# Kernel optimization log

Measured on AMD Instinct MI355X. Metric: run time of the kernel, lower is better.

The kernel has to match this reference:

```python
import jax, jax.numpy as jnp
import numpy as np

B, IN, COND, H, LAT, E, GH = 8192, 256, 1024, 1024, 128, 6, 64
INP = LAT + COND      # decoder layer0 input size = 1152
INTER = LAT + H       # decoder layer1/2 input size = 1152


def setup_inputs() -> dict:
    key = jax.random.key(0)
    ks = jax.random.split(key, 30)
    n = lambda k, shape, s=0.02: jax.random.normal(k, shape, dtype=jnp.float32) * s
    return {
        'x': jax.random.normal(ks[0], (B, IN), dtype=jnp.float32),
        'y': jax.random.normal(ks[1], (B, COND), dtype=jnp.float32),
        'eps': jax.random.normal(ks[2], (B, LAT), dtype=jnp.float32),
        # encoder: layer k input = prev_dim + IN (x is re-concatenated each layer)
        'enc_w0': n(ks[3], (IN + COND + IN, H)), 'enc_b0': jnp.zeros((H,), jnp.float32),
        'enc_w1': n(ks[4], (H + IN, H)),         'enc_b1': jnp.zeros((H,), jnp.float32),
        'mu_w': n(ks[5], (H, LAT)),  'mu_b': jnp.zeros((LAT,), jnp.float32),
        'lv_w': n(ks[6], (H, LAT)),  'lv_b': jnp.zeros((LAT,), jnp.float32),
        # gating network (input = latent + cond)
        'g_w0': n(ks[7], (INP, GH)), 'g_b0': jnp.zeros((GH,), jnp.float32),
        'g_w1': n(ks[8], (GH, GH)),  'g_b1': jnp.zeros((GH,), jnp.float32),
        'g_w2': n(ks[9], (GH, E)),   'g_b2': jnp.zeros((E,), jnp.float32),
        # expert weights [E, in, out] and biases [E, out] (bias init 0.01 as in source)
        'exp_w0': n(ks[10], (E, INP, H)),   'exp_b0': jnp.full((E, H), 0.01, jnp.float32),
        'exp_w1': n(ks[11], (E, INTER, H)), 'exp_b1': jnp.full((E, H), 0.01, jnp.float32),
        'exp_w2': n(ks[12], (E, INTER, IN)), 'exp_b2': jnp.full((E, IN), 0.01, jnp.float32),
    }


def _forward(x, y, eps, enc_w0, enc_b0, enc_w1, enc_b1, mu_w, mu_b, lv_w, lv_b,
             g_w0, g_b0, g_w1, g_b1, g_w2, g_b2,
             exp_w0, exp_b0, exp_w1, exp_b1, exp_w2, exp_b2):
    elu = jax.nn.elu
    # --- Encoder ---
    h = jnp.concatenate([x, y], axis=1)
    h = elu(jnp.concatenate([h, x], axis=1) @ enc_w0 + enc_b0)
    h = elu(jnp.concatenate([h, x], axis=1) @ enc_w1 + enc_b1)
    mu = h @ mu_w + mu_b
    logvar = h @ lv_w + lv_b
    # --- Reparameterize (eps passed explicitly for determinism) ---
    z = mu + eps * jnp.exp(0.5 * logvar)
    # --- MixedDecoder ---
    g = jnp.concatenate([z, y], axis=1)
    g = elu(g @ g_w0 + g_b0)
    g = elu(g @ g_w1 + g_b1)
    coeff = jax.nn.softmax(g @ g_w2 + g_b2, axis=1)  # [B, E]
    layer_out = y
    for W, bb, act in ((exp_w0, exp_b0, True), (exp_w1, exp_b1, True), (exp_w2, exp_b2, False)):
        inp = jnp.concatenate([z, layer_out], axis=1)  # [B, I]
        # fused mixture-of-experts projection: avoids materializing per-sample [B,I,O] weight
        out = coeff @ bb + jnp.einsum('be,bi,eio->bo', coeff, inp, W)
        layer_out = elu(out) if act else out
    return layer_out, mu, logvar


def reference(x, y, eps, enc_w0, enc_b0, enc_w1, enc_b1, mu_w, mu_b, lv_w, lv_b,
              g_w0, g_b0, g_w1, g_b1, g_w2, g_b2,
              exp_w0, exp_b0, exp_w1, exp_b1, exp_w2, exp_b2):
    return _forward(x, y, eps, enc_w0, enc_b0, enc_w1, enc_b1, mu_w, mu_b, lv_w, lv_b,
                    g_w0, g_b0, g_w1, g_b1, g_w2, g_b2,
                    exp_w0, exp_b0, exp_w1, exp_b1, exp_w2, exp_b2)
```

## Files before the change

### kernel.cpp

```cpp
#include <hip/hip_runtime.h>
#include <hip/hip_bf16.h>
#include <cstddef>

using u16 = unsigned short;
using short8 = __attribute__((ext_vector_type(8))) short;
using f32x4 = __attribute__((ext_vector_type(4))) float;

constexpr int B_   = 8192;
constexpr int IN_  = 256;
constexpr int COND_= 1024;
constexpr int H_   = 1024;
constexpr int LAT_ = 128;
constexpr int NE_  = 6;
constexpr int GH_  = 64;
constexpr int INP_ = 1152;
constexpr int K0_  = 1536;
constexpr int K1_  = 1280;

constexpr int BK = 64;

typedef const __attribute__((address_space(1))) void gv_t;
typedef __attribute__((address_space(3))) void lv_t;
#define GLDS(g, l) __builtin_amdgcn_global_load_lds((gv_t*)(g), (lv_t*)(l), 16, 0, 0)

__device__ __forceinline__ u16 f2b(float f) {
  __hip_bfloat16 h = __float2bfloat16(f);
  return *reinterpret_cast<u16*>(&h);
}
__device__ __forceinline__ float elu1(float x) { return x > 0.f ? x : (__expf(x) - 1.f); }

__global__ void k_transpose(const float* __restrict__ in, u16* __restrict__ out,
                            int R, int C, long inStride, long outStride) {
  __shared__ float t[32][33];
  const float* ip = in + (long)blockIdx.z * inStride;
  u16* op = out + (long)blockIdx.z * outStride;
  int c0 = blockIdx.x * 32, r0 = blockIdx.y * 32;
  int tx = threadIdx.x, ty = threadIdx.y;
#pragma unroll
  for (int i = 0; i < 4; i++) {
    int r = r0 + ty + i * 8, c = c0 + tx;
    if (r < R && c < C) t[ty + i * 8][tx] = ip[(long)r * C + c];
  }
  __syncthreads();
#pragma unroll
  for (int i = 0; i < 4; i++) {
    int c = c0 + ty + i * 8, r = r0 + tx;
    if (r < R && c < C) op[(long)c * R + r] = f2b(t[tx][ty + i * 8]);
  }
}

__global__ void k_prep(const float* __restrict__ x, const float* __restrict__ y,
                       u16* __restrict__ A0, u16* __restrict__ A1) {
  long idx = (long)blockIdx.x * blockDim.x + threadIdx.x;
  long n0 = (long)B_ * K0_;
  if (idx < n0) {
    int b = (int)(idx / K0_), c = (int)(idx % K0_);
    float v;
    if (c < IN_)            v = x[(long)b * IN_ + c];
    else if (c < IN_+COND_) v = y[(long)b * COND_ + (c - IN_)];
    else                    v = x[(long)b * IN_ + (c - IN_ - COND_)];
    A0[idx] = f2b(v);
  } else {
    long j = idx - n0;
    if (j < (long)B_ * IN_) {
      int b = (int)(j / IN_), c = (int)(j % IN_);
      A1[(long)b * K1_ + H_ + c] = f2b(x[(long)b * IN_ + c]);
    }
  }
}

__global__ void k_z(const float* __restrict__ mu, const float* __restrict__ lv,
                    const float* __restrict__ eps, const float* __restrict__ y,
                    u16* __restrict__ ZY, u16* __restrict__ D1, u16* __restrict__ D2) {
  long idx = (long)blockIdx.x * blockDim.x + threadIdx.x;
  if (idx >= (long)B_ * INP_) return;
  int b = (int)(idx / INP_), c = (int)(idx % INP_);
  if (c < LAT_) {
    long o = (long)b * LAT_ + c;
    float z = mu[o] + eps[o] * __expf(0.5f * lv[o]);
    u16 zb = f2b(z);
    ZY[idx] = zb; D1[idx] = zb; D2[idx] = zb;
  } else {
    ZY[idx] = f2b(y[(long)b * COND_ + (c - LAT_)]);
  }
}

__global__ __launch_bounds__(256) void k_gate(const float* __restrict__ G1,
    const float* __restrict__ w1, const float* __restrict__ b1,
    const float* __restrict__ w2, const float* __restrict__ b2,
    float* __restrict__ coeff) {
  __shared__ float W1[64][65];
  __shared__ float W2[64][8];
  __shared__ float B1[64], B2[8];
  int tid = threadIdx.x;
  for (int i = tid; i < 64 * 64; i += 256) W1[i >> 6][i & 63] = w1[i];
  for (int i = tid; i < 64 * 6; i += 256) W2[i / 6][i % 6] = w2[i];
  if (tid < 64) B1[tid] = b1[tid];
  if (tid < 8)  B2[tid] = (tid < 6) ? b2[tid] : 0.f;
  __syncthreads();
  int row = blockIdx.x * 256 + tid;
  const float* gr = G1 + (long)row * GH_;
  float g[64];
#pragma unroll
  for (int i = 0; i < 16; i++) {
    float4 v = *(const float4*)(gr + i * 4);
    g[i*4] = v.x; g[i*4+1] = v.y; g[i*4+2] = v.z; g[i*4+3] = v.w;
  }
  float lg[6];
#pragma unroll
  for (int e = 0; e < 6; e++) lg[e] = B2[e];
  for (int n = 0; n < 64; n++) {
    float s = B1[n];
#pragma unroll
    for (int k = 0; k < 64; k++) s += g[k] * W1[k][n];
    s = elu1(s);
#pragma unroll
    for (int e = 0; e < 6; e++) lg[e] += s * W2[n][e];
  }
  float m = lg[0];
#pragma unroll
  for (int e = 1; e < 6; e++) m = fmaxf(m, lg[e]);
  float p[6], sum = 0.f;
#pragma unroll
  for (int e = 0; e < 6; e++) { p[e] = __expf(lg[e] - m); sum += p[e]; }
  float inv = 1.f / sum;
#pragma unroll
  for (int e = 0; e < 6; e++) coeff[(long)row * 6 + e] = p[e] * inv;
}

template<int KSTEPS, int E, bool MOE>
__global__ __launch_bounds__(512, 2) void k_gemm8(
    const u16* __restrict__ A,
    const u16* __restrict__ WT,
    const float* __restrict__ bias,
    const float* __restrict__ coeff,
    int N,
    u16* __restrict__ outH, int ldo)
{
  constexpr int KK = KSTEPS * BK;
  constexpr int T = E * KSTEPS;
  __shared__ __align__(16) u16 As[3][256][BK];
  __shared__ __align__(16) u16 Bs[3][128][BK];
  __shared__ float Cf[MOE ? 256 : 1][8];

  const int tid = threadIdx.x;
  const int lane = tid & 63, w = tid >> 6;
  const int wr = w >> 1, wc = w & 1;
  const int lin = blockIdx.x + blockIdx.y * gridDim.x;
  const int rb  = (lin & 7) * 4 + ((lin >> 3) & 3);
  const int cp  = lin >> 5;
  const int brow = rb * 256, bcol = cp * 128;
  const int lr = lane & 15, hi = lane >> 4;
  const int lk = hi * 8;
  const int xsw = (lr & 7) << 3;

  if (MOE) {
    if (tid < 256) {
#pragma unroll
      for (int e2 = 0; e2 < 8; e2++)
        Cf[tid][e2] = (e2 < 6) ? coeff[(long)(brow + tid) * 6 + e2] : 0.f;
    }
    __syncthreads();
  }

  f32x4 acc[4][4];
#pragma unroll
  for (int m = 0; m < 4; m++)
#pragma unroll
    for (int n = 0; n < 4; n++)
#pragma unroll
      for (int r = 0; r < 4; r++) acc[m][n][r] = 0.f;
  f32x4 pacc[MOE ? 4 : 1][MOE ? 4 : 1];
  if constexpr (MOE) {
#pragma unroll
    for (int m = 0; m < 4; m++)
#pragma unroll
      for (int n = 0; n < 4; n++)
#pragma unroll
        for (int r = 0; r < 4; r++) pacc[m][n][r] = 0.f;
  }

  const int srow = w * 8 + (lane >> 3);
  const int sdst = (lane & 7) * 8;
  const int ssrc = ((lane & 7) ^ ((lane >> 3) & 7)) * 8;
  const u16* Asrc = A + (long)(brow + srow) * KK + ssrc;
  const u16* Bsrc = WT + (long)(bcol + srow) * KK + ssrc;

  auto STAGE_H = [&](int t2, int buf, int h) {
    const int e2 = (E == 1) ? 0 : (t2 / KSTEPS);
    int k2 = (E == 1) ? t2 : (t2 % KSTEPS);
    if (E > 1 && (e2 & 1)) k2 = KSTEPS - 1 - k2;
    const u16* ap = Asrc + (long)k2 * BK;
    const u16* bp = Bsrc + (long)e2 * ((long)N * KK) + (long)k2 * BK;
    GLDS(ap + (long)((h * 2 + 0) * 64) * KK, &As[buf][(h * 2 + 0) * 64 + srow][sdst]);
    GLDS(ap + (long)((h * 2 + 1) * 64) * KK, &As[buf][(h * 2 + 1) * 64 + srow][sdst]);
    GLDS(bp + (long)(h * 64) * KK,           &Bs[buf][h * 64 + srow][sdst]);
  };

  STAGE_H(0, 0, 0); STAGE_H(0, 0, 1);
  STAGE_H(1, 1, 0); STAGE_H(1, 1, 1);
  asm volatile("s_waitcnt vmcnt(6)" ::: "memory");
  asm volatile("s_barrier" ::: "memory");

  for (int t = 0; t < T; ++t) {
    const int cur = t % 3;
    const int nbuf = (t + 2) % 3;
    const bool do_stage = (t + 2 < T);

    {
      short8 af[4], bfr[4];
      const int cc = lk ^ xsw;
#pragma unroll
      for (int m = 0; m < 4; m++)
        af[m] = *(const short8*)&As[cur][wr * 64 + m * 16 + lr][cc];
#pragma unroll
      for (int n = 0; n < 4; n++)
        bfr[n] = *(const short8*)&Bs[cur][wc * 64 + n * 16 + lr][cc];
      if (do_stage) STAGE_H(t + 2, nbuf, 0);
      asm volatile("s_barrier" ::: "memory");
      __builtin_amdgcn_s_setprio(1);
#pragma unroll
      for (int m = 0; m < 4; m++)
#pragma unroll
        for (int n = 0; n < 4; n++) {
          if constexpr (MOE)
            pacc[m][n] = __builtin_amdgcn_mfma_f32_16x16x32_bf16(af[m], bfr[n], pacc[m][n], 0, 0, 0);
          else
            acc[m][n] = __builtin_amdgcn_mfma_f32_16x16x32_bf16(af[m], bfr[n], acc[m][n], 0, 0, 0);
        }
      __builtin_amdgcn_s_setprio(0);
      asm volatile("s_barrier" ::: "memory");
    }

    {
      short8 af[4], bfr[4];
      const int cc = (32 + lk) ^ xsw;
#pragma unroll
      for (int m = 0; m < 4; m++)
        af[m] = *(const short8*)&As[cur][wr * 64 + m * 16 + lr][cc];
#pragma unroll
      for (int n = 0; n < 4; n++)
        bfr[n] = *(const short8*)&Bs[cur][wc * 64 + n * 16 + lr][cc];
      if (do_stage) STAGE_H(t + 2, nbuf, 1);
      asm volatile("s_barrier" ::: "memory");
      __builtin_amdgcn_s_setprio(1);
#pragma unroll
      for (int m = 0; m < 4; m++)
#pragma unroll
        for (int n = 0; n < 4; n++) {
          if constexpr (MOE)
            pacc[m][n] = __builtin_amdgcn_mfma_f32_16x16x32_bf16(af[m], bfr[n], pacc[m][n], 0, 0, 0);
          else
            acc[m][n] = __builtin_amdgcn_mfma_f32_16x16x32_bf16(af[m], bfr[n], acc[m][n], 0, 0, 0);
        }
      __builtin_amdgcn_s_setprio(0);
      if (t + 1 < T) {
        if (do_stage) asm volatile("s_waitcnt vmcnt(6)" ::: "memory");
        else          asm volatile("s_waitcnt vmcnt(0)" ::: "memory");
      }
      asm volatile("s_barrier" ::: "memory");
    }

    if constexpr (MOE) {
      if ((t + 1) % KSTEPS == 0) {
        const int e = t / KSTEPS;
#pragma unroll
        for (int m = 0; m < 4; m++)
#pragma unroll
          for (int r = 0; r < 4; r++) {
            float c = Cf[wr * 64 + m * 16 + hi * 4 + r][e];
#pragma unroll
            for (int n = 0; n < 4; n++) acc[m][n][r] += c * pacc[m][n][r];
          }
        if (t + 1 < T) {
#pragma unroll
          for (int m = 0; m < 4; m++)
#pragma unroll
            for (int n = 0; n < 4; n++)
#pragma unroll
              for (int r = 0; r < 4; r++) pacc[m][n][r] = 0.f;
        }
      }
    }
  }

#pragma unroll
  for (int m = 0; m < 4; m++)
#pragma unroll
    for (int n = 0; n < 4; n++) {
      const int col = bcol + wc * 64 + n * 16 + lr;
#pragma unroll
      for (int r = 0; r < 4; r++) {
        const int rowl = wr * 64 + m * 16 + hi * 4 + r;
        const long row = brow + rowl;
        float v = acc[m][n][r];
        if constexpr (MOE) {
          float bv = 0.f;
#pragma unroll
          for (int e = 0; e < 6; e++) bv += Cf[rowl][e] * bias[(long)e * N + col];
          v += bv;
        } else {
          v += bias[col];
        }
        v = elu1(v);
        outH[row * (long)ldo + col] = f2b(v);
      }
    }
}

template<int MREP, bool MOE>
__global__ __launch_bounds__(256, 2) void k_gemm(
    const u16* __restrict__ A, int lda,
    const u16* __restrict__ WT, long wstride,
    const float* __restrict__ bias,
    const float* __restrict__ coeff,
    int N, int K, int E,
    u16* __restrict__ outH, float* __restrict__ outF, float* __restrict__ outF2,
    int ldo, int splitcol, const float* __restrict__ bias2, int act)
{
  constexpr int BMt = 32 * MREP;
  __shared__ __align__(16) u16 As[2][BMt][BK];
  __shared__ __align__(16) u16 Bs[2][128][BK];
  __shared__ float Cf[MOE ? BMt : 1][8];

  const int tid = threadIdx.x;
  const int lane = tid & 63, w = tid >> 6;
  const int wr = w >> 1, wc = w & 1;
  const int brow = blockIdx.x * BMt, bcol = blockIdx.y * 128;
  const int lr = lane & 15, hi = lane >> 4;
  const int lk = hi * 8;
  const int xsw = (lr & 7) << 3;

  if (MOE && tid < BMt) {
#pragma unroll
    for (int e2 = 0; e2 < 8; e2++)
      Cf[tid][e2] = (e2 < 6) ? coeff[(long)(brow + tid) * 6 + e2] : 0.f;
  }

  f32x4 acc[MREP][4];
#pragma unroll
  for (int m = 0; m < MREP; m++)
#pragma unroll
    for (int n = 0; n < 4; n++)
#pragma unroll
      for (int r = 0; r < 4; r++) acc[m][n][r] = 0.f;

  const int srow = w * 8 + (lane >> 3);
  const int sdst = (lane & 7) * 8;
  const int ssrc = ((lane & 7) ^ ((lane >> 3) & 7)) * 8;
  const u16* Asrc = A + (long)(brow + srow) * lda + ssrc;
  const u16* Bsrc = WT + (long)(bcol + srow) * K + ssrc;
  const int KSTEPS = K / BK;

  int cur = 0;
#pragma unroll
  for (int i = 0; i < BMt / 32; i++)
    GLDS(Asrc + (long)(i * 32) * lda, &As[0][i * 32 + srow][sdst]);
#pragma unroll
  for (int i = 0; i < 4; i++)
    GLDS(Bsrc + (long)(i * 32) * K, &Bs[0][i * 32 + srow][sdst]);

  for (int e = 0; e < E; ++e) {
    f32x4 pacc[MREP][4];
    if constexpr (MOE) {
#pragma unroll
      for (int m = 0; m < MREP; m++)
#pragma unroll
        for (int n = 0; n < 4; n++)
#pragma unroll
          for (int r = 0; r < 4; r++) pacc[m][n][r] = 0.f;
    }

    for (int kt = 0; kt < KSTEPS; ++kt) {
      __syncthreads();
      int ne = e, nk = kt + 1;
      if (nk == KSTEPS) { nk = 0; ne = e + 1; }
      if (ne < E) {
        const u16* ap = Asrc + (long)nk * BK;
        const u16* bp = Bsrc + (long)ne * wstride + (long)nk * BK;
#pragma unroll
        for (int i = 0; i < BMt / 32; i++)
          GLDS(ap + (long)(i * 32) * lda, &As[cur ^ 1][i * 32 + srow][sdst]);
#pragma unroll
        for (int i = 0; i < 4; i++)
          GLDS(bp + (long)(i * 32) * K, &Bs[cur ^ 1][i * 32 + srow][sdst]);
      }
#pragma unroll
      for (int kk = 0; kk < BK; kk += 32) {
        short8 af[MREP], bfr[4];
        const int cc = (kk + lk) ^ xsw;
#pragma unroll
        for (int m = 0; m < MREP; m++)
          af[m] = *(const short8*)&As[cur][wr * (16 * MREP) + m * 16 + lr][cc];
#pragma unroll
        for (int n = 0; n < 4; n++)
          bfr[n] = *(const short8*)&Bs[cur][wc * 64 + n * 16 + lr][cc];
#pragma unroll
        for (int m = 0; m < MREP; m++)
#pragma unroll
          for (int n = 0; n < 4; n++) {
            if constexpr (MOE)
              pacc[m][n] = __builtin_amdgcn_mfma_f32_16x16x32_bf16(af[m], bfr[n], pacc[m][n], 0, 0, 0);
            else
              acc[m][n] = __builtin_amdgcn_mfma_f32_16x16x32_bf16(af[m], bfr[n], acc[m][n], 0, 0, 0);
          }
      }
      cur ^= 1;
    }
    if constexpr (MOE) {
#pragma unroll
      for (int m = 0; m < MREP; m++)
#pragma unroll
        for (int r = 0; r < 4; r++) {
          float c = Cf[wr * (16 * MREP) + m * 16 + hi * 4 + r][e];
#pragma unroll
          for (int n = 0; n < 4; n++) acc[m][n][r] += c * pacc[m][n][r];
        }
    }
  }

#pragma unroll
  for (int m = 0; m < MREP; m++)
#pragma unroll
    for (int n = 0; n < 4; n++) {
      int col = bcol + wc * 64 + n * 16 + lr;
      if (col >= N) continue;
#pragma unroll
      for (int r = 0; r < 4; r++) {
        int rowl = wr * (16 * MREP) + m * 16 + hi * 4 + r;
        long row = brow + rowl;
        float v = acc[m][n][r];
        if constexpr (MOE) {
          float bv = 0.f;
#pragma unroll
          for (int e = 0; e < 6; e++) bv += Cf[rowl][e] * bias[(long)e * N + col];
          v += bv;
        } else {
          v += (col < splitcol) ? bias[col] : bias2[col - splitcol];
        }
        if (act) v = elu1(v);
        if (outH) outH[row * ldo + col] = f2b(v);
        else if (col < splitcol) outF[row * ldo + col] = v;
        else outF2[row * ldo + (col - splitcol)] = v;
      }
    }
}

extern "C" void kernel_launch(void* const* d_in, const int* in_sizes, int n_in,
                              void* d_out, int out_size, void* d_ws, size_t ws_size,
                              hipStream_t stream) {
  (void)in_sizes; (void)out_size;
  if (n_in < 23) return;
  const float* x      = (const float*)d_in[0];
  const float* y      = (const float*)d_in[1];
  const float* eps    = (const float*)d_in[2];
  const float* enc_w0 = (const float*)d_in[3];
  const float* enc_b0 = (const float*)d_in[4];
  const float* enc_w1 = (const float*)d_in[5];
  const float* enc_b1 = (const float*)d_in[6];
  const float* mu_w   = (const float*)d_in[7];
  const float* mu_b   = (const float*)d_in[8];
  const float* lv_w   = (const float*)d_in[9];
  const float* lv_b   = (const float*)d_in[10];
  const float* g_w0   = (const float*)d_in[11];
  const float* g_b0   = (const float*)d_in[12];
  const float* g_w1   = (const float*)d_in[13];
  const float* g_b1   = (const float*)d_in[14];
  const float* g_w2   = (const float*)d_in[15];
  const float* g_b2   = (const float*)d_in[16];
  const float* exp_w0 = (const float*)d_in[17];
  const float* exp_b0 = (const float*)d_in[18];
  const float* exp_w1 = (const float*)d_in[19];
  const float* exp_b1 = (const float*)d_in[20];
  const float* exp_w2 = (const float*)d_in[21];
  const float* exp_b2 = (const float*)d_in[22];

  char* ws = (char*)d_ws;
  size_t off = 0;
  auto alloc = [&](size_t bytes) -> void* {
    void* p = ws + off; off += (bytes + 255) & ~(size_t)255; return p;
  };
  u16* A0     = (u16*)alloc((size_t)B_ * K0_ * 2);
  u16* A1     = (u16*)alloc((size_t)B_ * K1_ * 2);
  u16* H2     = (u16*)alloc((size_t)B_ * H_ * 2);
  u16* ZY     = (u16*)alloc((size_t)B_ * INP_ * 2);
  u16* encw0T = (u16*)alloc((size_t)K0_ * H_ * 2);
  u16* encw1T = (u16*)alloc((size_t)K1_ * H_ * 2);
  u16* mulvT  = (u16*)alloc((size_t)256 * H_ * 2);
  u16* gw0T   = (u16*)alloc((size_t)GH_ * INP_ * 2);
  u16* ew0T   = (u16*)alloc((size_t)NE_ * H_ * INP_ * 2);
  if (ws_size < off) return;

  u16* D1 = A0;
  u16* D2 = A1;
  float* G1    = (float*)H2;
  float* COEFF = (float*)((char*)H2 + (size_t)B_ * GH_ * 4);
  u16* ew2T = (u16*)((char*)H2 + (size_t)4 * 1024 * 1024);
  u16* ew1T = ZY;

  float* outO = (float*)d_out;
  float* muO  = outO + (size_t)B_ * IN_;
  float* lvO  = muO + (size_t)B_ * LAT_;

  dim3 tb(32, 8);
  k_transpose<<<dim3(32, 48), tb, 0, stream>>>(enc_w0, encw0T, K0_, H_, 0, 0);
  k_transpose<<<dim3(32, 40), tb, 0, stream>>>(enc_w1, encw1T, K1_, H_, 0, 0);
  k_transpose<<<dim3(4, 32),  tb, 0, stream>>>(mu_w, mulvT, H_, LAT_, 0, 0);
  k_transpose<<<dim3(4, 32),  tb, 0, stream>>>(lv_w, mulvT + (size_t)LAT_ * H_, H_, LAT_, 0, 0);
  k_transpose<<<dim3(2, 36),  tb, 0, stream>>>(g_w0, gw0T, INP_, GH_, 0, 0);
  k_transpose<<<dim3(32, 36, NE_), tb, 0, stream>>>(exp_w0, ew0T, INP_, H_,
                                                    (long)INP_ * H_, (long)INP_ * H_);
  long npr = (long)B_ * K0_ + (long)B_ * IN_;
  k_prep<<<(int)((npr + 255) / 256), 256, 0, stream>>>(x, y, A0, A1);

  k_gemm8<K0_ / BK, 1, false><<<dim3(32, 8), 512, 0, stream>>>(A0, encw0T, enc_b0,
      nullptr, H_, A1, K1_);
  k_gemm8<K1_ / BK, 1, false><<<dim3(32, 8), 512, 0, stream>>>(A1, encw1T, enc_b1,
      nullptr, H_, H2, H_);
  k_gemm<2, false><<<dim3(B_ / 64, 2), 256, 0, stream>>>(H2, H_, mulvT, 0, mu_b, nullptr,
      256, H_, 1, nullptr, muO, lvO, LAT_, LAT_, lv_b, 0);

  k_transpose<<<dim3(8, 36, NE_), tb, 0, stream>>>(exp_w2, ew2T, INP_, IN_,
                                                   (long)INP_ * IN_, (long)INP_ * IN_);
  long nz = (long)B_ * INP_;
  k_z<<<(int)((nz + 255) / 256), 256, 0, stream>>>(muO, lvO, eps, y, ZY, D1, D2);

  k_gemm<2, false><<<dim3(B_ / 64, 1), 256, 0, stream>>>(ZY, INP_, gw0T, 0, g_b0, nullptr,
      GH_, INP_, 1, nullptr, G1, nullptr, GH_, GH_, nullptr, 1);
  k_gate<<<B_ / 256, 256, 0, stream>>>(G1, g_w1, g_b1, g_w2, g_b2, COEFF);

  k_gemm8<INP_ / BK, NE_, true><<<dim3(32, 8), 512, 0, stream>>>(ZY, ew0T, exp_b0,
      COEFF, H_, D1 + LAT_, INP_);
  k_transpose<<<dim3(32, 36, NE_), tb, 0, stream>>>(exp_w1, ew1T, INP_, H_,
                                                    (long)INP_ * H_, (long)INP_ * H_);
  k_gemm8<INP_ / BK, NE_, true><<<dim3(32, 8), 512, 0, stream>>>(D1, ew1T, exp_b1,
      COEFF, H_, D2 + LAT_, INP_);
  k_gemm<2, true><<<dim3(B_ / 64, 2), 256, 0, stream>>>(D2, INP_, ew2T, (long)IN_ * INP_,
      exp_b2, COEFF, IN_, INP_, NE_, nullptr, outO, nullptr, IN_, IN_, nullptr, 0);
}
```

Before: 564.5 us.

## Merge prep/transpose launches and triple-buffer small GEMMs with split barriers

Folds six weight transposes and the input prep into one launch (k_pre), and the exp_w2 transpose plus the z computation into another (k_mid), which cuts the launch count. Replaces the generic double-buffered k_gemm with k_m2. k_m2 has compile-time K and expert count, a three-stage LDS ring with explicit vmcnt waits and raw s_barriers, and MFMA priority raised with s_setprio. It also walks the K tiles in serpentine order across experts. The aim is to hide load latency and launch overhead, at the cost of hand-managed synchronisation that is more fragile.

```diff
diff --git a/kernel.cpp b/kernel.cpp
--- a/kernel.cpp
+++ b/kernel.cpp
@@ -49,39 +49,101 @@
   }
 }
 
-__global__ void k_prep(const float* __restrict__ x, const float* __restrict__ y,
-                       u16* __restrict__ A0, u16* __restrict__ A1) {
-  long idx = (long)blockIdx.x * blockDim.x + threadIdx.x;
-  long n0 = (long)B_ * K0_;
-  if (idx < n0) {
-    int b = (int)(idx / K0_), c = (int)(idx % K0_);
-    float v;
-    if (c < IN_)            v = x[(long)b * IN_ + c];
-    else if (c < IN_+COND_) v = y[(long)b * COND_ + (c - IN_)];
-    else                    v = x[(long)b * IN_ + (c - IN_ - COND_)];
-    A0[idx] = f2b(v);
+__global__ __launch_bounds__(256) void k_pre(
+    const float* __restrict__ enc_w0, const float* __restrict__ enc_w1,
+    const float* __restrict__ mu_w, const float* __restrict__ lv_w,
+    const float* __restrict__ g_w0, const float* __restrict__ exp_w0,
+    const float* __restrict__ x, const float* __restrict__ y,
+    u16* __restrict__ encw0T, u16* __restrict__ encw1T, u16* __restrict__ mulvT,
+    u16* __restrict__ gw0T, u16* __restrict__ ew0T,
+    u16* __restrict__ A0, u16* __restrict__ A1)
+{
+  __shared__ float t[32][33];
+  const int b = blockIdx.x;
+  const int tid = threadIdx.x;
+  const int tx = tid & 31, ty = tid >> 5;
+
+  auto tr = [&](const float* in, u16* out, int R, int C, int bx, int by) {
+    int c0 = bx * 32, r0 = by * 32;
+#pragma unroll
+    for (int i = 0; i < 4; i++) {
+      int r = r0 + ty + i * 8, c = c0 + tx;
+      if (r < R && c < C) t[ty + i * 8][tx] = in[(long)r * C + c];
+    }
+    __syncthreads();
+#pragma unroll
+    for (int i = 0; i < 4; i++) {
+      int c = c0 + ty + i * 8, r = r0 + tx;
+      if (r < R && c < C) out[(long)c * R + r] = f2b(t[tx][ty + i * 8]);
+    }
+  };
+
+  if (b < 1536)       { tr(enc_w0, encw0T, K0_, H_, b & 31, b >> 5); }
+  else if (b < 2816)  { int l = b - 1536; tr(enc_w1, encw1T, K1_, H_, l & 31, l >> 5); }
+  else if (b < 2944)  { int l = b - 2816; tr(mu_w, mulvT, H_, LAT_, l & 3, l >> 2); }
+  else if (b < 3072)  { int l = b - 2944; tr(lv_w, mulvT + (size_t)LAT_ * H_, H_, LAT_, l & 3, l >> 2); }
+  else if (b < 3144)  { int l = b - 3072; tr(g_w0, gw0T, INP_, GH_, l & 1, l >> 1); }
+  else if (b < 10056) {
+    int l = b - 3144, e = l / 1152, r2 = l % 1152;
+    tr(exp_w0 + (long)e * INP_ * H_, ew0T + (long)e * INP_ * H_, INP_, H_, r2 & 31, r2 >> 5);
   } else {
-    long j = idx - n0;
-    if (j < (long)B_ * IN_) {
-      int b = (int)(j / IN_), c = (int)(j % IN_);
-      A1[(long)b * K1_ + H_ + c] = f2b(x[(long)b * IN_ + c]);
-    }
-  }
-}
-
-__global__ void k_z(const float* __restrict__ mu, const float* __restrict__ lv,
-                    const float* __restrict__ eps, const float* __restrict__ y,
-                    u16* __restrict__ ZY, u16* __restrict__ D1, u16* __restrict__ D2) {
-  long idx = (long)blockIdx.x * blockDim.x + threadIdx.x;
-  if (idx >= (long)B_ * INP_) return;
-  int b = (int)(idx / INP_), c = (int)(idx % INP_);
-  if (c < LAT_) {
-    long o = (long)b * LAT_ + c;
-    float z = mu[o] + eps[o] * __expf(0.5f * lv[o]);
-    u16 zb = f2b(z);
-    ZY[idx] = zb; D1[idx] = zb; D2[idx] = zb;
+    long idx = (long)(b - 10056) * 256 + tid;
+    long n0 = (long)B_ * K0_;
+    if (idx < n0) {
+      int bb = (int)(idx / K0_), c = (int)(idx % K0_);
+      float v;
+      if (c < IN_)              v = x[(long)bb * IN_ + c];
+      else if (c < IN_ + COND_) v = y[(long)bb * COND_ + (c - IN_)];
+      else                      v = x[(long)bb * IN_ + (c - IN_ - COND_)];
+      A0[idx] = f2b(v);
+    } else {
+      long j = idx - n0;
+      if (j < (long)B_ * IN_) {
+        int bb = (int)(j / IN_), c = (int)(j % IN_);
+        A1[(long)bb * K1_ + H_ + c] = f2b(x[(long)bb * IN_ + c]);
+      }
+    }
+  }
+}
+
+__global__ __launch_bounds__(256) void k_mid(
+    const float* __restrict__ exp_w2, u16* __restrict__ ew2T,
+    const float* __restrict__ mu, const float* __restrict__ lv,
+    const float* __restrict__ eps, const float* __restrict__ y,
+    u16* __restrict__ ZY, u16* __restrict__ D1, u16* __restrict__ D2)
+{
+  __shared__ float t[32][33];
+  const int b = blockIdx.x;
+  const int tid = threadIdx.x;
+  if (b < 1728) {
+    const int tx = tid & 31, ty = tid >> 5;
+    int e = b / 288, r2 = b % 288;
+    const float* in = exp_w2 + (long)e * INP_ * IN_;
+    u16* out = ew2T + (long)e * INP_ * IN_;
+    int c0 = (r2 & 7) * 32, r0 = (r2 >> 3) * 32;
+#pragma unroll
+    for (int i = 0; i < 4; i++) {
+      int r = r0 + ty + i * 8, c = c0 + tx;
+      if (r < INP_ && c < IN_) t[ty + i * 8][tx] = in[(long)r * IN_ + c];
+    }
+    __syncthreads();
+#pragma unroll
+    for (int i = 0; i < 4; i++) {
+      int c = c0 + ty + i * 8, r = r0 + tx;
+      if (r < INP_ && c < IN_) out[(long)c * INP_ + r] = f2b(t[tx][ty + i * 8]);
+    }
   } else {
-    ZY[idx] = f2b(y[(long)b * COND_ + (c - LAT_)]);
+    long idx = (long)(b - 1728) * 256 + tid;
+    if (idx >= (long)B_ * INP_) return;
+    int bb = (int)(idx / INP_), c = (int)(idx % INP_);
+    if (c < LAT_) {
+      long o = (long)bb * LAT_ + c;
+      float z = mu[o] + eps[o] * __expf(0.5f * lv[o]);
+      u16 zb = f2b(z);
+      ZY[idx] = zb; D1[idx] = zb; D2[idx] = zb;
+    } else {
+      ZY[idx] = f2b(y[(long)bb * COND_ + (c - LAT_)]);
+    }
   }
 }
 
@@ -308,127 +370,170 @@
     }
 }
 
-template<int MREP, bool MOE>
-__global__ __launch_bounds__(256, 2) void k_gemm(
-    const u16* __restrict__ A, int lda,
-    const u16* __restrict__ WT, long wstride,
-    const float* __restrict__ bias,
+template<int KSTEPS, int E, bool MOE>
+__global__ __launch_bounds__(256, 2) void k_m2(
+    const u16* __restrict__ A,
+    const u16* __restrict__ WT,
+    const float* __restrict__ bias, const float* __restrict__ bias2,
     const float* __restrict__ coeff,
-    int N, int K, int E,
+    int N,
     u16* __restrict__ outH, float* __restrict__ outF, float* __restrict__ outF2,
-    int ldo, int splitcol, const float* __restrict__ bias2, int act)
+    int ldo, int splitcol, int act)
 {
-  constexpr int BMt = 32 * MREP;
-  __shared__ __align__(16) u16 As[2][BMt][BK];
-  __shared__ __align__(16) u16 Bs[2][128][BK];
-  __shared__ float Cf[MOE ? BMt : 1][8];
+  constexpr int KK = KSTEPS * BK;
+  constexpr int T = E * KSTEPS;
+  __shared__ __align__(16) u16 As[3][64][BK];
+  __shared__ __align__(16) u16 Bs[3][128][BK];
+  __shared__ float Cf[MOE ? 64 : 1][8];
 
   const int tid = threadIdx.x;
   const int lane = tid & 63, w = tid >> 6;
   const int wr = w >> 1, wc = w & 1;
-  const int brow = blockIdx.x * BMt, bcol = blockIdx.y * 128;
+  const int brow = blockIdx.x * 64, bcol = blockIdx.y * 128;
   const int lr = lane & 15, hi = lane >> 4;
   const int lk = hi * 8;
   const int xsw = (lr & 7) << 3;
 
-  if (MOE && tid < BMt) {
-#pragma unroll
-    for (int e2 = 0; e2 < 8; e2++)
-      Cf[tid][e2] = (e2 < 6) ? coeff[(long)(brow + tid) * 6 + e2] : 0.f;
-  }
-
-  f32x4 acc[MREP][4];
-#pragma unroll
-  for (int m = 0; m < MREP; m++)
+  if (MOE) {
+    if (tid < 64) {
+#pragma unroll
+      for (int e2 = 0; e2 < 8; e2++)
+        Cf[tid][e2] = (e2 < 6) ? coeff[(long)(brow + tid) * 6 + e2] : 0.f;
+    }
+    __syncthreads();
+  }
+
+  f32x4 acc[2][4];
+#pragma unroll
+  for (int m = 0; m < 2; m++)
 #pragma unroll
     for (int n = 0; n < 4; n++)
 #pragma unroll
       for (int r = 0; r < 4; r++) acc[m][n][r] = 0.f;
+  f32x4 pacc[MOE ? 2 : 1][MOE ? 4 : 1];
+  if constexpr (MOE) {
+#pragma unroll
+    for (int m = 0; m < 2; m++)
+#pragma unroll
+      for (int n = 0; n < 4; n++)
+#pragma unroll
+        for (int r = 0; r < 4; r++) pacc[m][n][r] = 0.f;
+  }
 
   const int srow = w * 8 + (lane >> 3);
   const int sdst = (lane & 7) * 8;
   const int ssrc = ((lane & 7) ^ ((lane >> 3) & 7)) * 8;
-  const u16* Asrc = A + (long)(brow + srow) * lda + ssrc;
-  const u16* Bsrc = WT + (long)(bcol + srow) * K + ssrc;
-  const int KSTEPS = K / BK;
-
-  int cur = 0;
-#pragma unroll
-  for (int i = 0; i < BMt / 32; i++)
-    GLDS(Asrc + (long)(i * 32) * lda, &As[0][i * 32 + srow][sdst]);
-#pragma unroll
-  for (int i = 0; i < 4; i++)
-    GLDS(Bsrc + (long)(i * 32) * K, &Bs[0][i * 32 + srow][sdst]);
-
-  for (int e = 0; e < E; ++e) {
-    f32x4 pacc[MREP][4];
+  const u16* Asrc = A + (long)(brow + srow) * KK + ssrc;
+  const u16* Bsrc = WT + (long)(bcol + srow) * KK + ssrc;
+
+  auto STAGE_H = [&](int t2, int buf, int h) {
+    const int e2 = (E == 1) ? 0 : (t2 / KSTEPS);
+    int k2 = (E == 1) ? t2 : (t2 % KSTEPS);
+    if (E > 1 && (e2 & 1)) k2 = KSTEPS - 1 - k2;
+    const u16* ap = Asrc + (long)k2 * BK;
+    const u16* bp = Bsrc + (long)e2 * ((long)N * KK) + (long)k2 * BK;
+    GLDS(ap + (long)(h * 32) * KK,            &As[buf][h * 32 + srow][sdst]);
+    GLDS(bp + (long)(h * 64) * KK,            &Bs[buf][h * 64 + srow][sdst]);
+    GLDS(bp + (long)(h * 64 + 32) * KK,       &Bs[buf][h * 64 + 32 + srow][sdst]);
+  };
+
+  STAGE_H(0, 0, 0); STAGE_H(0, 0, 1);
+  STAGE_H(1, 1, 0); STAGE_H(1, 1, 1);
+  asm volatile("s_waitcnt vmcnt(6)" ::: "memory");
+  asm volatile("s_barrier" ::: "memory");
+
+  for (int t = 0; t < T; ++t) {
+    const int cur = t % 3;
+    const int nbuf = (t + 2) % 3;
+    const bool do_stage = (t + 2 < T);
+
+    {
+      short8 af[2], bfr[4];
+      const int cc = lk ^ xsw;
+#pragma unroll
+      for (int m = 0; m < 2; m++)
+        af[m] = *(const short8*)&As[cur][wr * 32 + m * 16 + lr][cc];
+#pragma unroll
+      for (int n = 0; n < 4; n++)
+        bfr[n] = *(const short8*)&Bs[cur][wc * 64 + n * 16 + lr][cc];
+      if (do_stage) STAGE_H(t + 2, nbuf, 0);
+      asm volatile("s_barrier" ::: "memory");
+      __builtin_amdgcn_s_setprio(1);
+#pragma unroll
+      for (int m = 0; m < 2; m++)
+#pragma unroll
+        for (int n = 0; n < 4; n++) {
+          if constexpr (MOE)
+            pacc[m][n] = __builtin_amdgcn_mfma_f32_16x16x32_bf16(af[m], bfr[n], pacc[m][n], 0, 0, 0);
+          else
+            acc[m][n] = __builtin_amdgcn_mfma_f32_16x16x32_bf16(af[m], bfr[n], acc[m][n], 0, 0, 0);
+        }
+      __builtin_amdgcn_s_setprio(0);
+      asm volatile("s_barrier" ::: "memory");
+    }
+
+    {
+      short8 af[2], bfr[4];
+      const int cc = (32 + lk) ^ xsw;
+#pragma unroll
+      for (int m = 0; m < 2; m++)
+        af[m] = *(const short8*)&As[cur][wr * 32 + m * 16 + lr][cc];
+#pragma unroll
+      for (int n = 0; n < 4; n++)
+        bfr[n] = *(const short8*)&Bs[cur][wc * 64 + n * 16 + lr][cc];
+      if (do_stage) STAGE_H(t + 2, nbuf, 1);
+      asm volatile("s_barrier" ::: "memory");
+      __builtin_amdgcn_s_setprio(1);
+#pragma unroll
+      for (int m = 0; m < 2; m++)
+#pragma unroll
+        for (int n = 0; n < 4; n++) {
+          if constexpr (MOE)
+            pacc[m][n] = __builtin_amdgcn_mfma_f32_16x16x32_bf16(af[m], bfr[n], pacc[m][n], 0, 0, 0);
+          else
+            acc[m][n] = __builtin_amdgcn_mfma_f32_16x16x32_bf16(af[m], bfr[n], acc[m][n], 0, 0, 0);
+        }
+      __builtin_amdgcn_s_setprio(0);
+      if (t + 1 < T) {
+        if (do_stage) asm volatile("s_waitcnt vmcnt(6)" ::: "memory");
+        else          asm volatile("s_waitcnt vmcnt(0)" ::: "memory");
+      }
+      asm volatile("s_barrier" ::: "memory");
+    }
+
     if constexpr (MOE) {
-#pragma unroll
-      for (int m = 0; m < MREP; m++)
-#pragma unroll
-        for (int n = 0; n < 4; n++)
-#pragma unroll
-          for (int r = 0; r < 4; r++) pacc[m][n][r] = 0.f;
-    }
-
-    for (int kt = 0; kt < KSTEPS; ++kt) {
-      __syncthreads();
-      int ne = e, nk = kt + 1;
-      if (nk == KSTEPS) { nk = 0; ne = e + 1; }
-      if (ne < E) {
-        const u16* ap = Asrc + (long)nk * BK;
-        const u16* bp = Bsrc + (long)ne * wstride + (long)nk * BK;
-#pragma unroll
-        for (int i = 0; i < BMt / 32; i++)
-          GLDS(ap + (long)(i * 32) * lda, &As[cur ^ 1][i * 32 + srow][sdst]);
-#pragma unroll
-        for (int i = 0; i < 4; i++)
-          GLDS(bp + (long)(i * 32) * K, &Bs[cur ^ 1][i * 32 + srow][sdst]);
+      if ((t + 1) % KSTEPS == 0) {
+        const int e = t / KSTEPS;
+#pragma unroll
+        for (int m = 0; m < 2; m++)
+#pragma unroll
+          for (int r = 0; r < 4; r++) {
+            float c = Cf[wr * 32 + m * 16 + hi * 4 + r][e];
+#pragma unroll
+            for (int n = 0; n < 4; n++) acc[m][n][r] += c * pacc[m][n][r];
+          }
+        if (t + 1 < T) {
+#pragma unroll
+          for (int m = 0; m < 2; m++)
+#pragma unroll
+            for (int n = 0; n < 4; n++)
+#pragma unroll
+              for (int r = 0; r < 4; r++) pacc[m][n][r] = 0.f;
+        }
       }
-#pragma unroll
-      for (int kk = 0; kk < BK; kk += 32) {
-        short8 af[MREP], bfr[4];
-        const int cc = (kk + lk) ^ xsw;
-#pragma unroll
-        for (int m = 0; m < MREP; m++)
-          af[m] = *(const short8*)&As[cur][wr * (16 * MREP) + m * 16 + lr][cc];
-#pragma unroll
-        for (int n = 0; n < 4; n++)
-          bfr[n] = *(const short8*)&Bs[cur][wc * 64 + n * 16 + lr][cc];
-#pragma unroll
-        for (int m = 0; m < MREP; m++)
-#pragma unroll
-          for (int n = 0; n < 4; n++) {
-            if constexpr (MOE)
-              pacc[m][n] = __builtin_amdgcn_mfma_f32_16x16x32_bf16(af[m], bfr[n], pacc[m][n], 0, 0, 0);
-            else
-              acc[m][n] = __builtin_amdgcn_mfma_f32_16x16x32_bf16(af[m], bfr[n], acc[m][n], 0, 0, 0);
-          }
-      }
-      cur ^= 1;
-    }
-    if constexpr (MOE) {
-#pragma unroll
-      for (int m = 0; m < MREP; m++)
-#pragma unroll
-        for (int r = 0; r < 4; r++) {
-          float c = Cf[wr * (16 * MREP) + m * 16 + hi * 4 + r][e];
-#pragma unroll
-          for (int n = 0; n < 4; n++) acc[m][n][r] += c * pacc[m][n][r];
-        }
-    }
-  }
-
-#pragma unroll
-  for (int m = 0; m < MREP; m++)
+    }
+  }
+
+#pragma unroll
+  for (int m = 0; m < 2; m++)
 #pragma unroll
     for (int n = 0; n < 4; n++) {
-      int col = bcol + wc * 64 + n * 16 + lr;
+      const int col = bcol + wc * 64 + n * 16 + lr;
       if (col >= N) continue;
 #pragma unroll
       for (int r = 0; r < 4; r++) {
-        int rowl = wr * (16 * MREP) + m * 16 + hi * 4 + r;
-        long row = brow + rowl;
+        const int rowl = wr * 32 + m * 16 + hi * 4 + r;
+        const long row = brow + rowl;
         float v = acc[m][n][r];
         if constexpr (MOE) {
           float bv = 0.f;
@@ -439,9 +544,9 @@
           v += (col < splitcol) ? bias[col] : bias2[col - splitcol];
         }
         if (act) v = elu1(v);
-        if (outH) outH[row * ldo + col] = f2b(v);
-        else if (col < splitcol) outF[row * ldo + col] = v;
-        else outF2[row * ldo + (col - splitcol)] = v;
+        if (outH) outH[row * (long)ldo + col] = f2b(v);
+        else if (col < splitcol) outF[row * (long)ldo + col] = v;
+        else outF2[row * (long)ldo + (col - splitcol)] = v;
       }
     }
 }
@@ -502,39 +607,29 @@
   float* muO  = outO + (size_t)B_ * IN_;
   float* lvO  = muO + (size_t)B_ * LAT_;
 
-  dim3 tb(32, 8);
-  k_transpose<<<dim3(32, 48), tb, 0, stream>>>(enc_w0, encw0T, K0_, H_, 0, 0);
-  k_transpose<<<dim3(32, 40), tb, 0, stream>>>(enc_w1, encw1T, K1_, H_, 0, 0);
-  k_transpose<<<dim3(4, 32),  tb, 0, stream>>>(mu_w, mulvT, H_, LAT_, 0, 0);
-  k_transpose<<<dim3(4, 32),  tb, 0, stream>>>(lv_w, mulvT + (size_t)LAT_ * H_, H_, LAT_, 0, 0);
-  k_transpose<<<dim3(2, 36),  tb, 0, stream>>>(g_w0, gw0T, INP_, GH_, 0, 0);
-  k_transpose<<<dim3(32, 36, NE_), tb, 0, stream>>>(exp_w0, ew0T, INP_, H_,
-                                                    (long)INP_ * H_, (long)INP_ * H_);
-  long npr = (long)B_ * K0_ + (long)B_ * IN_;
-  k_prep<<<(int)((npr + 255) / 256), 256, 0, stream>>>(x, y, A0, A1);
+  k_pre<<<67400, 256, 0, stream>>>(enc_w0, enc_w1, mu_w, lv_w, g_w0, exp_w0,
+      x, y, encw0T, encw1T, mulvT, gw0T, ew0T, A0, A1);
 
   k_gemm8<K0_ / BK, 1, false><<<dim3(32, 8), 512, 0, stream>>>(A0, encw0T, enc_b0,
       nullptr, H_, A1, K1_);
   k_gemm8<K1_ / BK, 1, false><<<dim3(32, 8), 512, 0, stream>>>(A1, encw1T, enc_b1,
       nullptr, H_, H2, H_);
-  k_gemm<2, false><<<dim3(B_ / 64, 2), 256, 0, stream>>>(H2, H_, mulvT, 0, mu_b, nullptr,
-      256, H_, 1, nullptr, muO, lvO, LAT_, LAT_, lv_b, 0);
-
-  k_transpose<<<dim3(8, 36, NE_), tb, 0, stream>>>(exp_w2, ew2T, INP_, IN_,
-                                                   (long)INP_ * IN_, (long)INP_ * IN_);
-  long nz = (long)B_ * INP_;
-  k_z<<<(int)((nz + 255) / 256), 256, 0, stream>>>(muO, lvO, eps, y, ZY, D1, D2);
-
-  k_gemm<2, false><<<dim3(B_ / 64, 1), 256, 0, stream>>>(ZY, INP_, gw0T, 0, g_b0, nullptr,
-      GH_, INP_, 1, nullptr, G1, nullptr, GH_, GH_, nullptr, 1);
+
+  k_m2<H_ / BK, 1, false><<<dim3(B_ / 64, 2), 256, 0, stream>>>(H2, mulvT,
+      mu_b, lv_b, nullptr, 256, nullptr, muO, lvO, LAT_, LAT_, 0);
+
+  k_mid<<<38592, 256, 0, stream>>>(exp_w2, ew2T, muO, lvO, eps, y, ZY, D1, D2);
+
+  k_m2<INP_ / BK, 1, false><<<dim3(B_ / 64, 1), 256, 0, stream>>>(ZY, gw0T,
+      g_b0, g_b0, nullptr, GH_, nullptr, G1, nullptr, GH_, GH_, 1);
   k_gate<<<B_ / 256, 256, 0, stream>>>(G1, g_w1, g_b1, g_w2, g_b2, COEFF);
 
   k_gemm8<INP_ / BK, NE_, true><<<dim3(32, 8), 512, 0, stream>>>(ZY, ew0T, exp_b0,
       COEFF, H_, D1 + LAT_, INP_);
-  k_transpose<<<dim3(32, 36, NE_), tb, 0, stream>>>(exp_w1, ew1T, INP_, H_,
+  k_transpose<<<dim3(32, 36, NE_), dim3(32, 8), 0, stream>>>(exp_w1, ew1T, INP_, H_,
                                                     (long)INP_ * H_, (long)INP_ * H_);
   k_gemm8<INP_ / BK, NE_, true><<<dim3(32, 8), 512, 0, stream>>>(D1, ew1T, exp_b1,
       COEFF, H_, D2 + LAT_, INP_);
-  k_gemm<2, true><<<dim3(B_ / 64, 2), 256, 0, stream>>>(D2, INP_, ew2T, (long)IN_ * INP_,
-      exp_b2, COEFF, IN_, INP_, NE_, nullptr, outO, nullptr, IN_, IN_, nullptr, 0);
-}
+  k_m2<INP_ / BK, NE_, true><<<dim3(B_ / 64, 2), 256, 0, stream>>>(D2, ew2T,
+      exp_b2, nullptr, COEFF, IN_, nullptr, outO, nullptr, IN_, IN_, 0);
+}
```

Measured after the change: 533.5 us. 5.5% less time.
